# Performance work log

Hardware: AMD Instinct MI355X
Metric: run time of the kernel (lower is better)

## Reference

```python
import jax, jax.numpy as jnp
import numpy as np

L, D, H, V, BS = 12, 768, 12, 50257, 1024  # n_layer, n_embd, n_head, vocab, block_size
B, T = 2, 1024
HD = D // H
SCALE = HD ** -0.5


def setup_inputs() -> dict:
    key = jax.random.key(0)
    ks = jax.random.split(key, 10)
    s = 0.02  # init std from _init_weights
    f = lambda k, shape: jax.random.normal(k, shape, jnp.float32) * s
    return {
        "idx": jax.random.randint(ks[0], (B, T), 0, V),
        "tok_emb": f(ks[1], (V, D)),          # tied with LM head
        "pos_emb": f(ks[2], (BS, D)),
        "wqkv": f(ks[3], (L, 3 * D, D)), "bqkv": jnp.zeros((L, 3 * D), jnp.float32),
        "wproj": f(ks[4], (L, D, D)),    "bproj": jnp.zeros((L, D), jnp.float32),
        "ln1_g": jnp.ones((L, D), jnp.float32), "ln1_b": jnp.zeros((L, D), jnp.float32),
        "ln2_g": jnp.ones((L, D), jnp.float32), "ln2_b": jnp.zeros((L, D), jnp.float32),
        "w1": f(ks[5], (L, 4 * D, D)), "b1": jnp.zeros((L, 4 * D), jnp.float32),
        "w2": f(ks[6], (L, D, 4 * D)), "b2": jnp.zeros((L, D), jnp.float32),
        "lnf_g": jnp.ones((D,), jnp.float32), "lnf_b": jnp.zeros((D,), jnp.float32),
    }


def _ln(x, g, b, eps=1e-5):
    mu = jnp.mean(x, axis=-1, keepdims=True)
    var = jnp.mean(jnp.square(x - mu), axis=-1, keepdims=True)
    return (x - mu) * jax.lax.rsqrt(var + eps) * g + b


def _gpt_forward(idx, tok_emb, pos_emb, wqkv, bqkv, wproj, bproj,
                 ln1_g, ln1_b, ln2_g, ln2_b, w1, b1, w2, b2, lnf_g, lnf_b):
    Bb, Tt = idx.shape
    x = tok_emb[idx] + pos_emb[:Tt]  # [B,T,D]; dropout=0 in eval
    causal = jnp.tril(jnp.ones((Tt, Tt), bool))

    def block(x, p):
        wq, bq, wp, bp, g1, be1, g2, be2, W1, B1, W2, B2 = p
        h = _ln(x, g1, be1)
        qkv = h @ wq.T + bq                       # [B,T,3D]
        q, k, v = jnp.split(qkv, 3, axis=-1)
        to_heads = lambda z: z.reshape(Bb, Tt, H, HD).transpose(0, 2, 1, 3)
        q, k, v = to_heads(q), to_heads(k), to_heads(v)
        att = jnp.einsum('bhqd,bhkd->bhqk', q, k) * SCALE
        att = jnp.where(causal, att, -jnp.inf)
        att = jax.nn.softmax(att, axis=-1)
        y = jnp.einsum('bhqk,bhkd->bhqd', att, v)
        y = y.transpose(0, 2, 1, 3).reshape(Bb, Tt, D)
        x = x + (y @ wp.T + bp)
        h2 = _ln(x, g2, be2)
        ff = jax.nn.gelu(h2 @ W1.T + B1, approximate=False) @ W2.T + B2
        return x + ff, None

    layer_params = (wqkv, bqkv, wproj, bproj, ln1_g, ln1_b, ln2_g, ln2_b, w1, b1, w2, b2)
    x, _ = jax.lax.scan(block, x, layer_params)
    x = _ln(x, lnf_g, lnf_b)
    return x @ tok_emb.T  # tied LM head, [B,T,V]


def reference(idx, tok_emb, pos_emb, wqkv, bqkv, wproj, bproj,
              ln1_g, ln1_b, ln2_g, ln2_b, w1, b1, w2, b2, lnf_g, lnf_b):
    return _gpt_forward(idx, tok_emb, pos_emb, wqkv, bqkv, wproj, bproj,
                        ln1_g, ln1_b, ln2_g, ln2_b, w1, b1, w2, b2, lnf_g, lnf_b)
```

## Files before the change

### kernel.cpp

```cpp
#include <hip/hip_runtime.h>
#include <hip/hip_bf16.h>

#define TT 1024
#define DD 768
#define HH 12
#define LL 12
#define VV 50257
#define MROWS 2048

typedef __attribute__((ext_vector_type(4))) float f32x4;
typedef __attribute__((ext_vector_type(8))) short bf16x8;

__device__ __forceinline__ short f2bf(float f) {
  __hip_bfloat16 h = __float2bfloat16(f);
  short s;
  __builtin_memcpy(&s, &h, 2);
  return s;
}

__device__ __forceinline__ void gload16(const void* g, void* l) {
  __builtin_amdgcn_global_load_lds(
      (const __attribute__((address_space(1))) unsigned int*)g,
      (__attribute__((address_space(3))) unsigned int*)l, 16, 0, 0);
}

__device__ __forceinline__ float wsum(float v) {
#pragma unroll
  for (int o = 32; o; o >>= 1) v += __shfl_xor(v, o, 64);
  return v;
}

__global__ __launch_bounds__(256) void cvt_k(const float* __restrict__ src,
                                             short* __restrict__ dst, long n4)
{
  const long stride = (long)gridDim.x * 256;
  for (long i = (long)blockIdx.x * 256 + threadIdx.x; i < n4; i += stride) {
    const float4 v = ((const float4*)src)[i];
    short4 h;
    h.x = f2bf(v.x); h.y = f2bf(v.y); h.z = f2bf(v.z); h.w = f2bf(v.w);
    ((short4*)dst)[i] = h;
  }
}

__global__ __launch_bounds__(256) void embed_k(const int* __restrict__ idx,
    const float* __restrict__ tok, const float* __restrict__ pos,
    float* __restrict__ x)
{
  int i = blockIdx.x * 256 + threadIdx.x;
  int d = i % DD;
  int bt = i / DD;
  int t = bt & (TT - 1);
  x[i] = tok[(long)idx[bt] * DD + d] + pos[t * DD + d];
}

__global__ __launch_bounds__(256) void ln_k(const float* __restrict__ x,
    const float* __restrict__ g, const float* __restrict__ b,
    short* __restrict__ out)
{
  const int row = blockIdx.x;
  const float* xr = x + (long)row * DD;
  float vals[3];
  float s = 0.f, s2 = 0.f;
#pragma unroll
  for (int i = 0; i < 3; ++i) {
    float v = xr[threadIdx.x + i * 256];
    vals[i] = v; s += v; s2 += v * v;
  }
  __shared__ float rs[4], rs2[4];
  s = wsum(s); s2 = wsum(s2);
  if (!(threadIdx.x & 63)) { rs[threadIdx.x >> 6] = s; rs2[threadIdx.x >> 6] = s2; }
  __syncthreads();
  s  = rs[0] + rs[1] + rs[2] + rs[3];
  s2 = rs2[0] + rs2[1] + rs2[2] + rs2[3];
  const float mu = s * (1.f / DD);
  const float var = s2 * (1.f / DD) - mu * mu;
  const float rstd = rsqrtf(var + 1e-5f);
#pragma unroll
  for (int i = 0; i < 3; ++i) {
    int d = threadIdx.x + i * 256;
    out[(long)row * DD + d] = f2bf((vals[i] - mu) * rstd * g[d] + b[d]);
  }
}

__global__ __launch_bounds__(256) void vtrans_k(const short* __restrict__ qkv,
                                                short* __restrict__ vt)
{
  const int tt = blockIdx.x;
  const int z  = blockIdx.y;
  const int zb = z / HH, zh = z % HH;
  __shared__ short tile[64][65];
  for (int e = threadIdx.x; e < 64 * 64; e += 256) {
    int lt = e >> 6, d = e & 63;
    tile[lt][d] = qkv[(long)(zb * TT + tt * 64 + lt) * (3 * DD) + 2 * DD + zh * 64 + d];
  }
  __syncthreads();
  for (int e = threadIdx.x; e < 64 * 64; e += 256) {
    int d = e >> 6, lt = e & 63;
    vt[((long)z * 64 + d) * TT + tt * 64 + lt] = tile[lt][d];
  }
}

__global__ __launch_bounds__(256) void flash_k(const short* __restrict__ qkv,
                                               const short* __restrict__ vt,
                                               short* __restrict__ y)
{
  const int qt = (int)gridDim.x - 1 - (int)blockIdx.x;
  const int z  = blockIdx.y;
  const int zb = z / HH, zh = z % HH;
  const int w    = threadIdx.x >> 6;
  const int lane = threadIdx.x & 63;
  const int c = lane & 15, g = lane >> 4;

  __shared__ short Pl[4][16][40];
  __shared__ float Ol[4][16][64];
  __shared__ float ml[4][16], ll[4][16];

  const int qbase = qt * 16;
  const long rowQ = (long)(zb * TT + qbase + c) * (3 * DD) + zh * 64;

  bf16x8 qf[2];
  qf[0] = *(const bf16x8*)(qkv + rowQ + g * 8);
  qf[1] = *(const bf16x8*)(qkv + rowQ + 32 + g * 8);

  f32x4 O[4] = {};
  f32x4 mrun, lrun;
#pragma unroll
  for (int r = 0; r < 4; ++r) { mrun[r] = -1e30f; lrun[r] = 0.f; }

  const float CSC = 0.125f * 1.44269504089f;
  const int nt = (qbase + 15) / 32 + 1;

  for (int t = w; t < nt; t += 4) {
    const int k0 = t * 32;
    f32x4 acc[2] = {};
#pragma unroll
    for (int nf = 0; nf < 2; ++nf) {
      const long rowK = (long)(zb * TT + k0 + nf * 16 + c) * (3 * DD) + DD + zh * 64;
      bf16x8 kf0 = *(const bf16x8*)(qkv + rowK + g * 8);
      bf16x8 kf1 = *(const bf16x8*)(qkv + rowK + 32 + g * 8);
      acc[nf] = __builtin_amdgcn_mfma_f32_16x16x32_bf16(qf[0], kf0, acc[nf], 0, 0, 0);
      acc[nf] = __builtin_amdgcn_mfma_f32_16x16x32_bf16(qf[1], kf1, acc[nf], 0, 0, 0);
    }
    f32x4 tv[2];
    const int mask_needed = (k0 + 31 > qbase);
#pragma unroll
    for (int nf = 0; nf < 2; ++nf) {
      const int k_abs = k0 + nf * 16 + c;
#pragma unroll
      for (int r = 0; r < 4; ++r) {
        float val = acc[nf][r] * CSC;
        if (mask_needed && k_abs > qbase + g * 4 + r) val = -1e30f;
        tv[nf][r] = val;
      }
    }
    f32x4 rmax;
#pragma unroll
    for (int r = 0; r < 4; ++r) rmax[r] = fmaxf(tv[0][r], tv[1][r]);
#pragma unroll
    for (int off = 1; off < 16; off <<= 1) {
#pragma unroll
      for (int r = 0; r < 4; ++r) rmax[r] = fmaxf(rmax[r], __shfl_xor(rmax[r], off, 64));
    }
    f32x4 mnew, rfac;
#pragma unroll
    for (int r = 0; r < 4; ++r) {
      mnew[r] = fmaxf(mrun[r], rmax[r]);
      rfac[r] = exp2f(mrun[r] - mnew[r]);
      mrun[r] = mnew[r];
    }
    f32x4 e0, e1, rsum;
#pragma unroll
    for (int r = 0; r < 4; ++r) {
      e0[r] = exp2f(tv[0][r] - mnew[r]);
      e1[r] = exp2f(tv[1][r] - mnew[r]);
      rsum[r] = e0[r] + e1[r];
    }
#pragma unroll
    for (int off = 1; off < 16; off <<= 1) {
#pragma unroll
      for (int r = 0; r < 4; ++r) rsum[r] += __shfl_xor(rsum[r], off, 64);
    }
#pragma unroll
    for (int r = 0; r < 4; ++r) lrun[r] = lrun[r] * rfac[r] + rsum[r];
#pragma unroll
    for (int nf = 0; nf < 4; ++nf)
#pragma unroll
      for (int r = 0; r < 4; ++r) O[nf][r] *= rfac[r];
#pragma unroll
    for (int r = 0; r < 4; ++r) {
      Pl[w][g * 4 + r][c]      = f2bf(e0[r]);
      Pl[w][g * 4 + r][16 + c] = f2bf(e1[r]);
    }
    asm volatile("s_waitcnt lgkmcnt(0)" ::: "memory");
    const bf16x8 pf = *(const bf16x8*)&Pl[w][c][g * 8];
#pragma unroll
    for (int nf = 0; nf < 4; ++nf) {
      const bf16x8 vf = *(const bf16x8*)(vt + ((long)z * 64 + nf * 16 + c) * TT + k0 + g * 8);
      O[nf] = __builtin_amdgcn_mfma_f32_16x16x32_bf16(pf, vf, O[nf], 0, 0, 0);
    }
  }

#pragma unroll
  for (int nf = 0; nf < 4; ++nf)
#pragma unroll
    for (int r = 0; r < 4; ++r)
      Ol[w][g * 4 + r][nf * 16 + c] = O[nf][r];
  if (c == 0) {
#pragma unroll
    for (int r = 0; r < 4; ++r) { ml[w][g * 4 + r] = mrun[r]; ll[w][g * 4 + r] = lrun[r]; }
  }
  __syncthreads();

  for (int e = threadIdx.x; e < 16 * 64; e += 256) {
    const int row = e >> 6, d = e & 63;
    const float M = fmaxf(fmaxf(ml[0][row], ml[1][row]), fmaxf(ml[2][row], ml[3][row]));
    float L = 0.f, Ov = 0.f;
#pragma unroll
    for (int u = 0; u < 4; ++u) {
      const float f = exp2f(ml[u][row] - M);
      L += ll[u][row] * f;
      Ov += Ol[u][row][d] * f;
    }
    y[(long)(zb * TT + qbase + row) * DD + zh * 64 + d] = f2bf(Ov / L);
  }
}

template<int BM, int BN, int BK, typename TB, int EPI, bool LMSWZ, bool PIPE>
__global__ __launch_bounds__(256) void gemm_nt(
    const short* __restrict__ A, const TB* __restrict__ Bm,
    const float* __restrict__ bias, const float* __restrict__ resid,
    void* __restrict__ Cout,
    int M, int N, int K, int lda, int ldb, int ldc,
    long aSB, long aSH, long bSB, long bSH, long cSB, long cSH,
    float scale, int causal)
{
  int n0, m0;
  if constexpr (LMSWZ) {
    const int l = blockIdx.x;
    const int x = l & 7;
    const int j = l >> 3;
    const int mt = j & 15;
    const int nl = j >> 4;
    const int npan = (N + BN - 1) / BN;
    const int q = npan >> 3, rr = npan & 7;
    const int cnt = q + (x < rr);
    if (nl >= cnt) return;
    const int nstart = x * q + (x < rr ? x : rr);
    n0 = (nstart + nl) * BN;
    m0 = mt * BM;
  } else {
    n0 = blockIdx.x * BN;
    m0 = blockIdx.y * BM;
  }
  if (causal && n0 >= m0 + BM) return;
  const int z = blockIdx.z;
  const int zb = z / HH, zh = z % HH;
  const short* Ag = A + zb * aSB + zh * aSH + (long)m0 * lda;
  const TB*    Bg = Bm + zb * bSB + zh * bSH;
  const long  cOff = zb * cSB + zh * cSH;

  constexpr int NBUF = PIPE ? 2 : 1;
  __shared__ __align__(16) short Als[NBUF][BM][BK];
  __shared__ __align__(16) short Bls[NBUF][BN][BK];

  const int tid = threadIdx.x;
  const int lane = tid & 63, wid = tid >> 6;
  constexpr int WTM = BM / 2, WTN = BN / 2;
  constexpr int FM = WTM / 16, FN = WTN / 16;
  const int wr = wid >> 1, wc = wid & 1;

  f32x4 acc[FM][FN] = {};
  const int kAoff = (lane >> 4) * 8;
  constexpr bool B_IS_F32 = (sizeof(TB) == 4);
  constexpr int CPR = BK / 8;
  constexpr int NCA = BM * CPR;
  constexpr int NCB = BN * CPR;
  constexpr int IA = NCA / 256, IB = NCB / 256;
  constexpr int GPT = IA + IB;
  static_assert(CPR == 8, "swizzle assumes 128B rows (BK=64)");
  static_assert(B_IS_F32 || (NCA % 256 == 0 && NCB % 256 == 0), "chunk grid");

  auto compute = [&](int buf) {
#pragma unroll
    for (int kk = 0; kk < BK; kk += 32) {
      bf16x8 af[FM], bfr[FN];
#pragma unroll
      for (int mi = 0; mi < FM; ++mi) {
        const int Ra = wr * WTM + mi * 16 + (lane & 15);
        const int kca = (kk + kAoff) >> 3;
        af[mi] = *(const bf16x8*)&Als[buf][Ra][(kca ^ (Ra & 7)) << 3];
      }
#pragma unroll
      for (int ni = 0; ni < FN; ++ni) {
        const int Rb = wc * WTN + ni * 16 + (lane & 15);
        const int kcb = (kk + kAoff) >> 3;
        bfr[ni] = *(const bf16x8*)&Bls[buf][Rb][(kcb ^ (Rb & 7)) << 3];
      }
#pragma unroll
      for (int mi = 0; mi < FM; ++mi)
#pragma unroll
        for (int ni = 0; ni < FN; ++ni)
          acc[mi][ni] = __builtin_amdgcn_mfma_f32_16x16x32_bf16(af[mi], bfr[ni], acc[mi][ni], 0, 0, 0);
    }
  };

  if constexpr (!B_IS_F32) {
    const short* ap[IA];
    const short* bp[IB];
#pragma unroll
    for (int i = 0; i < IA; ++i) {
      const int cch = i * 256 + tid;
      const int r = cch / CPR, kc = cch % CPR;
      ap[i] = Ag + (long)r * lda + ((kc ^ (r & 7)) << 3);
    }
#pragma unroll
    for (int i = 0; i < IB; ++i) {
      const int cch = i * 256 + tid;
      const int r = cch / CPR, kc = cch % CPR;
      int gr = n0 + r; gr = (gr < N) ? gr : (N - 1);
      bp[i] = (const short*)Bg + (long)gr * ldb + ((kc ^ (r & 7)) << 3);
    }
    const int ldsoff = wid * 64 * 16;

    auto stage = [&](int buf) {
#pragma unroll
      for (int i = 0; i < IA; ++i) {
        gload16(ap[i], (char*)&Als[buf][0][0] + i * 4096 + ldsoff);
        ap[i] += BK;
      }
#pragma unroll
      for (int i = 0; i < IB; ++i) {
        gload16(bp[i], (char*)&Bls[buf][0][0] + i * 4096 + ldsoff);
        bp[i] += BK;
      }
    };

    if constexpr (PIPE) {
      const int KT = K / BK;
      stage(0);
      for (int kt = 0; kt < KT; ++kt) {
        const int cur = kt & 1;
        if (kt + 1 < KT) {
          stage(cur ^ 1);
          asm volatile("s_waitcnt vmcnt(%0)" :: "i"(GPT));
        } else {
          asm volatile("s_waitcnt vmcnt(0)");
        }
        __builtin_amdgcn_sched_barrier(0);
        __builtin_amdgcn_s_barrier();
        __builtin_amdgcn_sched_barrier(0);
        compute(cur);
        asm volatile("" ::: "memory");
        __builtin_amdgcn_s_barrier();
        __builtin_amdgcn_sched_barrier(0);
      }
    } else {
      const int KT = K / BK;
      for (int kt = 0; kt < KT; ++kt) {
        stage(0);
        __syncthreads();
        compute(0);
        __syncthreads();
      }
    }
  } else {
    for (int k0 = 0; k0 < K; k0 += BK) {
#pragma unroll
      for (int cc = tid; cc < BM * (BK / 8); cc += 256) {
        int r = cc / (BK / 8), kc = cc % (BK / 8);
        const uint4 v = *(const uint4*)(Ag + (long)r * lda + k0 + kc * 8);
        *(uint4*)((char*)&Als[0][r][0] + ((kc ^ (r & 7)) << 4)) = v;
      }
#pragma unroll
      for (int cc = tid; cc < BN * (BK / 4); cc += 256) {
        int r = cc / (BK / 4), kc = cc % (BK / 4);
        int gr = n0 + r; gr = (gr < N) ? gr : (N - 1);
        const float4 v = *(const float4*)((const float*)Bg + (long)gr * ldb + k0 + kc * 4);
        short4 h4;
        h4.x = f2bf(v.x); h4.y = f2bf(v.y); h4.z = f2bf(v.z); h4.w = f2bf(v.w);
        *(short4*)((char*)&Bls[0][r][0] + ((kc * 8) ^ ((r & 7) << 4))) = h4;
      }
      __syncthreads();
      compute(0);
      __syncthreads();
    }
  }

  const int rq = (lane >> 4) << 2;
  const int cl = lane & 15;
#pragma unroll
  for (int mi = 0; mi < FM; ++mi) {
#pragma unroll
    for (int ni = 0; ni < FN; ++ni) {
      const int cg = n0 + wc * WTN + ni * 16 + cl;
      if (cg >= N) continue;
      const int rbase = m0 + wr * WTM + mi * 16 + rq;
#pragma unroll
      for (int q = 0; q < 4; ++q) {
        const long cidx = cOff + (long)(rbase + q) * ldc + cg;
        const float v = acc[mi][ni][q];
        if constexpr (EPI == 0) {
          ((float*)Cout)[cidx] = v * scale;
        } else if constexpr (EPI == 1) {
          ((short*)Cout)[cidx] = f2bf(v + bias[cg]);
        } else if constexpr (EPI == 2) {
          ((float*)Cout)[cidx] = resid[cidx] + v + bias[cg];
        } else if constexpr (EPI == 3) {
          const float zz = v + bias[cg];
          ((short*)Cout)[cidx] = f2bf(0.5f * zz * (1.f + erff(zz * 0.70710678118f)));
        } else {
          ((short*)Cout)[cidx] = f2bf(v);
        }
      }
    }
  }
}

template<typename TB>
static void run_model(const int* idx, const float* tok_f, const float* pos,
                      const TB* wqkv, const float* bqkv, const TB* wproj, const float* bproj,
                      const float* ln1g, const float* ln1b, const float* ln2g, const float* ln2b,
                      const TB* w1, const float* b1, const TB* w2, const float* b2,
                      const float* lnfg, const float* lnfb, const TB* tok_w,
                      float* xa, float* xb, short* hbf, short* qkv, short* vt,
                      short* ybf, short* ffb,
                      float* out, hipStream_t stream)
{
  embed_k<<<dim3(MROWS * DD / 256), 256, 0, stream>>>(idx, tok_f, pos, xa);

  float* xc = xa;
  float* xn = xb;
  for (int l = 0; l < LL; ++l) {
    ln_k<<<dim3(MROWS), 256, 0, stream>>>(xc, ln1g + l * DD, ln1b + l * DD, hbf);
    gemm_nt<128, 64, 64, TB, 1, false, true><<<dim3(36, 16, 1), 256, 0, stream>>>(
        hbf, wqkv + (long)l * 3 * DD * DD, bqkv + l * 3 * DD, nullptr, qkv,
        MROWS, 3 * DD, DD, DD, DD, 3 * DD, 0, 0, 0, 0, 0, 0, 1.f, 0);
    vtrans_k<<<dim3(16, 24), 256, 0, stream>>>(qkv, vt);
    flash_k<<<dim3(64, 24), 256, 0, stream>>>(qkv, vt, ybf);
    gemm_nt<64, 64, 64, TB, 2, false, true><<<dim3(12, 32, 1), 256, 0, stream>>>(
        ybf, wproj + (long)l * DD * DD, bproj + l * DD, xc, xn,
        MROWS, DD, DD, DD, DD, DD, 0, 0, 0, 0, 0, 0, 1.f, 0);
    ln_k<<<dim3(MROWS), 256, 0, stream>>>(xn, ln2g + l * DD, ln2b + l * DD, hbf);
    gemm_nt<128, 64, 64, TB, 3, false, true><<<dim3(48, 16, 1), 256, 0, stream>>>(
        hbf, w1 + (long)l * 4 * DD * DD, b1 + l * 4 * DD, nullptr, ffb,
        MROWS, 4 * DD, DD, DD, DD, 4 * DD, 0, 0, 0, 0, 0, 0, 1.f, 0);
    gemm_nt<64, 64, 64, TB, 2, false, true><<<dim3(12, 32, 1), 256, 0, stream>>>(
        ffb, w2 + (long)l * DD * 4 * DD, b2 + l * DD, xn, xc,
        MROWS, DD, 4 * DD, 4 * DD, 4 * DD, DD, 0, 0, 0, 0, 0, 0, 1.f, 0);
  }
  ln_k<<<dim3(MROWS), 256, 0, stream>>>(xc, lnfg, lnfb, hbf);
  gemm_nt<128, 128, 64, TB, 0, true, false><<<dim3(6400, 1, 1), 256, 0, stream>>>(
      hbf, tok_w, nullptr, nullptr, out,
      MROWS, VV, DD, DD, DD, VV, 0, 0, 0, 0, 0, 0, 1.f, 0);
}

extern "C" void kernel_launch(void* const* d_in, const int* in_sizes, int n_in,
                              void* d_out, int out_size, void* d_ws, size_t ws_size,
                              hipStream_t stream)
{
  const int*   idx  = (const int*)d_in[0];
  const float* tok  = (const float*)d_in[1];
  const float* pos  = (const float*)d_in[2];
  const float* wqkv = (const float*)d_in[3];
  const float* bqkv = (const float*)d_in[4];
  const float* wproj= (const float*)d_in[5];
  const float* bproj= (const float*)d_in[6];
  const float* ln1g = (const float*)d_in[7];
  const float* ln1b = (const float*)d_in[8];
  const float* ln2g = (const float*)d_in[9];
  const float* ln2b = (const float*)d_in[10];
  const float* w1   = (const float*)d_in[11];
  const float* b1   = (const float*)d_in[12];
  const float* w2   = (const float*)d_in[13];
  const float* b2   = (const float*)d_in[14];
  const float* lnfg = (const float*)d_in[15];
  const float* lnfb = (const float*)d_in[16];
  float* out = (float*)d_out;

  const long E_WQKV = (long)LL * 3 * DD * DD;
  const long E_WPRJ = (long)LL * DD * DD;
  const long E_W1   = (long)LL * 4 * DD * DD;
  const long E_W2   = E_W1;
  const long E_TOK  = (long)VV * DD;
  const long E_WSUM = E_WQKV + E_WPRJ + E_W1 + E_W2 + E_TOK;

  const size_t NEED_B = 44040192;
  const size_t NEED_A = NEED_B + 2 * (size_t)E_WSUM;

  if (ws_size < NEED_B) return;
  const bool bf16w = (ws_size >= NEED_A);

  char* ws = (char*)d_ws;
  short *wqkv_h = nullptr, *wprj_h = nullptr, *w1_h = nullptr, *w2_h = nullptr, *tok_h = nullptr;
  if (bf16w) {
    wqkv_h = (short*)ws; ws += E_WQKV * 2;
    wprj_h = (short*)ws; ws += E_WPRJ * 2;
    w1_h   = (short*)ws; ws += E_W1 * 2;
    w2_h   = (short*)ws; ws += E_W2 * 2;
    tok_h  = (short*)ws; ws += E_TOK * 2;
  }
  float* xa  = (float*)ws; ws += (size_t)MROWS * DD * 4;
  float* xb  = (float*)ws; ws += (size_t)MROWS * DD * 4;
  short* hbf = (short*)ws; ws += (size_t)MROWS * DD * 2;
  short* qkv = (short*)ws; ws += (size_t)MROWS * 3 * DD * 2;
  short* vt  = (short*)ws; ws += (size_t)24 * 64 * TT * 2;
  short* ybf = (short*)ws; ws += (size_t)MROWS * DD * 2;
  short* ffb = (short*)ws; ws += (size_t)MROWS * 4 * DD * 2;

  if (bf16w) {
    cvt_k<<<dim3(2048), 256, 0, stream>>>(wqkv, wqkv_h, E_WQKV / 4);
    cvt_k<<<dim3(2048), 256, 0, stream>>>(wproj, wprj_h, E_WPRJ / 4);
    cvt_k<<<dim3(2048), 256, 0, stream>>>(w1, w1_h, E_W1 / 4);
    cvt_k<<<dim3(2048), 256, 0, stream>>>(w2, w2_h, E_W2 / 4);
    cvt_k<<<dim3(2048), 256, 0, stream>>>(tok, tok_h, E_TOK / 4);
    run_model<short>(idx, tok, pos, wqkv_h, bqkv, wprj_h, bproj,
                     ln1g, ln1b, ln2g, ln2b, w1_h, b1, w2_h, b2, lnfg, lnfb, tok_h,
                     xa, xb, hbf, qkv, vt, ybf, ffb, out, stream);
  } else {
    run_model<float>(idx, tok, pos, wqkv, bqkv, wproj, bproj,
                     ln1g, ln1b, ln2g, ln2b, w1, b1, w2, b2, lnfg, lnfb, tok,
                     xa, xb, hbf, qkv, vt, ybf, ffb, out, stream);
  }
}
```

Measured before the change: 2.275 ms.

## Fuse V transpose into QKV GEMM epilogue and use warp-per-row LayerNorm

Adds a QKV GEMM epilogue that writes the V section directly into the transposed per-head layout, which removes the separate vtrans kernel launch and its round-trip through global memory. LayerNorm now assigns one wavefront per row with float4 loads and short4 stores, so the shared-memory reduction and block barrier go away. The grid for the weight-conversion kernel is also doubled. The fused epilogue hard-codes the batch/time bit layout and passes the vt buffer through the float resid pointer.

```diff
diff --git a/kernel.cpp b/kernel.cpp
--- a/kernel.cpp
+++ b/kernel.cpp
@@ -57,46 +57,31 @@
     const float* __restrict__ g, const float* __restrict__ b,
     short* __restrict__ out)
 {
-  const int row = blockIdx.x;
+  const int w = threadIdx.x >> 6;
+  const int lane = threadIdx.x & 63;
+  const int row = blockIdx.x * 4 + w;
   const float* xr = x + (long)row * DD;
-  float vals[3];
+  float4 v[3];
   float s = 0.f, s2 = 0.f;
 #pragma unroll
   for (int i = 0; i < 3; ++i) {
-    float v = xr[threadIdx.x + i * 256];
-    vals[i] = v; s += v; s2 += v * v;
-  }
-  __shared__ float rs[4], rs2[4];
+    v[i] = ((const float4*)xr)[lane + i * 64];
+    s  += v[i].x + v[i].y + v[i].z + v[i].w;
+    s2 += v[i].x * v[i].x + v[i].y * v[i].y + v[i].z * v[i].z + v[i].w * v[i].w;
+  }
   s = wsum(s); s2 = wsum(s2);
-  if (!(threadIdx.x & 63)) { rs[threadIdx.x >> 6] = s; rs2[threadIdx.x >> 6] = s2; }
-  __syncthreads();
-  s  = rs[0] + rs[1] + rs[2] + rs[3];
-  s2 = rs2[0] + rs2[1] + rs2[2] + rs2[3];
   const float mu = s * (1.f / DD);
   const float var = s2 * (1.f / DD) - mu * mu;
   const float rstd = rsqrtf(var + 1e-5f);
 #pragma unroll
   for (int i = 0; i < 3; ++i) {
-    int d = threadIdx.x + i * 256;
-    out[(long)row * DD + d] = f2bf((vals[i] - mu) * rstd * g[d] + b[d]);
-  }
-}
-
-__global__ __launch_bounds__(256) void vtrans_k(const short* __restrict__ qkv,
-                                                short* __restrict__ vt)
-{
-  const int tt = blockIdx.x;
-  const int z  = blockIdx.y;
-  const int zb = z / HH, zh = z % HH;
-  __shared__ short tile[64][65];
-  for (int e = threadIdx.x; e < 64 * 64; e += 256) {
-    int lt = e >> 6, d = e & 63;
-    tile[lt][d] = qkv[(long)(zb * TT + tt * 64 + lt) * (3 * DD) + 2 * DD + zh * 64 + d];
-  }
-  __syncthreads();
-  for (int e = threadIdx.x; e < 64 * 64; e += 256) {
-    int d = e >> 6, lt = e & 63;
-    vt[((long)z * 64 + d) * TT + tt * 64 + lt] = tile[lt][d];
+    const int d0 = (lane + i * 64) * 4;
+    short4 h;
+    h.x = f2bf((v[i].x - mu) * rstd * g[d0 + 0] + b[d0 + 0]);
+    h.y = f2bf((v[i].y - mu) * rstd * g[d0 + 1] + b[d0 + 1]);
+    h.z = f2bf((v[i].z - mu) * rstd * g[d0 + 2] + b[d0 + 2]);
+    h.w = f2bf((v[i].w - mu) * rstd * g[d0 + 3] + b[d0 + 3]);
+    ((short4*)(out + (long)row * DD))[lane + i * 64] = h;
   }
 }
 
@@ -395,6 +380,25 @@
       const int cg = n0 + wc * WTN + ni * 16 + cl;
       if (cg >= N) continue;
       const int rbase = m0 + wr * WTM + mi * 16 + rq;
+      if constexpr (EPI == 5) {
+        if (cg >= 2 * DD) {
+          const int hh = (cg - 2 * DD) >> 6, dd2 = (cg - 2 * DD) & 63;
+          const int bI = rbase >> 10, tI = rbase & (TT - 1);
+          const float bv = bias[cg];
+          short4 h4;
+          h4.x = f2bf(acc[mi][ni][0] + bv);
+          h4.y = f2bf(acc[mi][ni][1] + bv);
+          h4.z = f2bf(acc[mi][ni][2] + bv);
+          h4.w = f2bf(acc[mi][ni][3] + bv);
+          short* vtp = (short*)(void*)resid;
+          *(short4*)(vtp + (((long)(bI * HH + hh) * 64 + dd2) << 10) + tI) = h4;
+        } else {
+#pragma unroll
+          for (int q = 0; q < 4; ++q)
+            ((short*)Cout)[(long)(rbase + q) * ldc + cg] = f2bf(acc[mi][ni][q] + bias[cg]);
+        }
+        continue;
+      }
 #pragma unroll
       for (int q = 0; q < 4; ++q) {
         const long cidx = cOff + (long)(rbase + q) * ldc + cg;
@@ -431,16 +435,15 @@
   float* xc = xa;
   float* xn = xb;
   for (int l = 0; l < LL; ++l) {
-    ln_k<<<dim3(MROWS), 256, 0, stream>>>(xc, ln1g + l * DD, ln1b + l * DD, hbf);
-    gemm_nt<128, 64, 64, TB, 1, false, true><<<dim3(36, 16, 1), 256, 0, stream>>>(
-        hbf, wqkv + (long)l * 3 * DD * DD, bqkv + l * 3 * DD, nullptr, qkv,
+    ln_k<<<dim3(MROWS / 4), 256, 0, stream>>>(xc, ln1g + l * DD, ln1b + l * DD, hbf);
+    gemm_nt<128, 64, 64, TB, 5, false, true><<<dim3(36, 16, 1), 256, 0, stream>>>(
+        hbf, wqkv + (long)l * 3 * DD * DD, bqkv + l * 3 * DD, (const float*)vt, qkv,
         MROWS, 3 * DD, DD, DD, DD, 3 * DD, 0, 0, 0, 0, 0, 0, 1.f, 0);
-    vtrans_k<<<dim3(16, 24), 256, 0, stream>>>(qkv, vt);
     flash_k<<<dim3(64, 24), 256, 0, stream>>>(qkv, vt, ybf);
     gemm_nt<64, 64, 64, TB, 2, false, true><<<dim3(12, 32, 1), 256, 0, stream>>>(
         ybf, wproj + (long)l * DD * DD, bproj + l * DD, xc, xn,
         MROWS, DD, DD, DD, DD, DD, 0, 0, 0, 0, 0, 0, 1.f, 0);
-    ln_k<<<dim3(MROWS), 256, 0, stream>>>(xn, ln2g + l * DD, ln2b + l * DD, hbf);
+    ln_k<<<dim3(MROWS / 4), 256, 0, stream>>>(xn, ln2g + l * DD, ln2b + l * DD, hbf);
     gemm_nt<128, 64, 64, TB, 3, false, true><<<dim3(48, 16, 1), 256, 0, stream>>>(
         hbf, w1 + (long)l * 4 * DD * DD, b1 + l * 4 * DD, nullptr, ffb,
         MROWS, 4 * DD, DD, DD, DD, 4 * DD, 0, 0, 0, 0, 0, 0, 1.f, 0);
@@ -448,7 +451,7 @@
         ffb, w2 + (long)l * DD * 4 * DD, b2 + l * DD, xn, xc,
         MROWS, DD, 4 * DD, 4 * DD, 4 * DD, DD, 0, 0, 0, 0, 0, 0, 1.f, 0);
   }
-  ln_k<<<dim3(MROWS), 256, 0, stream>>>(xc, lnfg, lnfb, hbf);
+  ln_k<<<dim3(MROWS / 4), 256, 0, stream>>>(xc, lnfg, lnfb, hbf);
   gemm_nt<128, 128, 64, TB, 0, true, false><<<dim3(6400, 1, 1), 256, 0, stream>>>(
       hbf, tok_w, nullptr, nullptr, out,
       MROWS, VV, DD, DD, DD, VV, 0, 0, 0, 0, 0, 0, 1.f, 0);
@@ -508,11 +511,11 @@
   short* ffb = (short*)ws; ws += (size_t)MROWS * 4 * DD * 2;
 
   if (bf16w) {
-    cvt_k<<<dim3(2048), 256, 0, stream>>>(wqkv, wqkv_h, E_WQKV / 4);
-    cvt_k<<<dim3(2048), 256, 0, stream>>>(wproj, wprj_h, E_WPRJ / 4);
-    cvt_k<<<dim3(2048), 256, 0, stream>>>(w1, w1_h, E_W1 / 4);
-    cvt_k<<<dim3(2048), 256, 0, stream>>>(w2, w2_h, E_W2 / 4);
-    cvt_k<<<dim3(2048), 256, 0, stream>>>(tok, tok_h, E_TOK / 4);
+    cvt_k<<<dim3(4096), 256, 0, stream>>>(wqkv, wqkv_h, E_WQKV / 4);
+    cvt_k<<<dim3(4096), 256, 0, stream>>>(wproj, wprj_h, E_WPRJ / 4);
+    cvt_k<<<dim3(4096), 256, 0, stream>>>(w1, w1_h, E_W1 / 4);
+    cvt_k<<<dim3(4096), 256, 0, stream>>>(w2, w2_h, E_W2 / 4);
+    cvt_k<<<dim3(4096), 256, 0, stream>>>(tok, tok_h, E_TOK / 4);
     run_model<short>(idx, tok, pos, wqkv_h, bqkv, wprj_h, bproj,
                      ln1g, ln1b, ln2g, ln2b, w1_h, b1, w2_h, b2, lnfg, lnfb, tok_h,
                      xa, xb, hbf, qkv, vt, ybf, ffb, out, stream);
```

New measurement: 2.231 ms. No clear change (-1.9%).
